# Kernel tuning notes

Hardware: AMD Instinct MI355X
Metric: run time of the kernel (lower is better)

The kernel has to match this reference:

```python
import jax, jax.numpy as jnp
import numpy as np

N_NODES = 10000
LN_EPS = 1e-5


def _gcn(x, W, b, src, dst):
    # GraphConvolution: linear transform then sum-aggregate messages over edges.
    sup = x @ W                               # [B, N, H]
    msg = sup[:, src, :]                      # [B, E, H] gather from source nodes
    agg = jax.vmap(lambda m: jax.ops.segment_sum(m, dst, num_segments=N_NODES))(msg)
    return agg + b


def _layernorm(x, g, b):
    mu = jnp.mean(x, axis=-1, keepdims=True)
    var = jnp.var(x, axis=-1, keepdims=True)
    return (x - mu) * jax.lax.rsqrt(var + LN_EPS) * g + b


def _attention_pool(x, W, u, num_iterations=3):
    # x: [B, N, d] -> r: [B, 1, d]
    a = jnp.tanh(x @ W) @ u                   # [B, N]
    alpha = jax.nn.softmax(a, axis=1)
    r = jnp.einsum('bn,bnd->bd', alpha, x)
    for _ in range(num_iterations):
        beta = jax.nn.softmax(jnp.einsum('bnd,bd->bn', x, r), axis=1)
        r = jnp.einsum('bn,bnd->bd', beta, x)
    return r[:, None, :]


def _forward(x, src, dst, W_conv0, b_conv0, W_convs, b_convs,
             mW1, mb1, mW2, mb2, mW3, mb3,
             ln1_g, ln1_b, ln2_g, ln2_b, attnW, attnu, fW1, fb1, fW2, fb2,
             fcW, fcb):
    gelu = lambda t: jax.nn.gelu(t, approximate=False)
    # stacked GCN layers (first layer distinct input dim)
    x = gelu(_gcn(x, W_conv0, b_conv0, src, dst))
    for i in range(W_convs.shape[0]):
        x = gelu(_gcn(x, W_convs[i], b_convs[i], src, dst))
    # dropout is identity in eval mode
    # MLP head
    x = jax.nn.relu(x @ mW1 + mb1)
    x = jax.nn.relu(x @ mW2 + mb2)
    x = x @ mW3 + mb3
    # Encoder: 2 layers of (attention-pool residual + LN + FFN residual + LN)
    for i in range(2):
        x = x + _attention_pool(x, attnW[i], attnu[i])   # broadcast [B,1,d]
        x = _layernorm(x, ln1_g[i], ln1_b[i])
        h = jax.nn.relu(x @ fW1[i] + fb1[i]) @ fW2[i] + fb2[i]
        x = _layernorm(x + h, ln2_g[i], ln2_b[i])
    x = x @ fcW + fcb                          # [B, N, out]
    return x.mean(axis=1)                      # [B, out]


def setup_inputs() -> dict:
    key = jax.random.key(0)
    ks = jax.random.split(key, 32)
    B, N, E = 4, N_NODES, 160000
    F_in, H, D, A, OUT = 128, 256, 256, 8, 10
    s = lambda k, *shape: jax.random.normal(k, shape, jnp.float32) * 0.05
    return {
        'x': jax.random.normal(ks[0], (B, N, F_in), jnp.float32),
        'src': jax.random.randint(ks[1], (E,), 0, N, jnp.int32),
        'dst': jax.random.randint(ks[2], (E,), 0, N, jnp.int32),
        'W_conv0': s(ks[3], F_in, H), 'b_conv0': s(ks[4], H),
        'W_convs': s(ks[5], 3, H, H), 'b_convs': s(ks[6], 3, H),
        'mW1': s(ks[7], H, H // 2), 'mb1': s(ks[8], H // 2),
        'mW2': s(ks[9], H // 2, H // 4), 'mb2': s(ks[10], H // 4),
        'mW3': s(ks[11], H // 4, D), 'mb3': s(ks[12], D),
        'ln1_g': jnp.ones((2, D), jnp.float32), 'ln1_b': jnp.zeros((2, D), jnp.float32),
        'ln2_g': jnp.ones((2, D), jnp.float32), 'ln2_b': jnp.zeros((2, D), jnp.float32),
        'attnW': s(ks[13], 2, D, A), 'attnu': s(ks[14], 2, A),
        'fW1': s(ks[15], 2, D, H), 'fb1': s(ks[16], 2, H),
        'fW2': s(ks[17], 2, H, D), 'fb2': s(ks[18], 2, D),
        'fcW': s(ks[19], D, OUT), 'fcb': s(ks[20], OUT),
    }


def reference(x, src, dst, W_conv0, b_conv0, W_convs, b_convs,
              mW1, mb1, mW2, mb2, mW3, mb3,
              ln1_g, ln1_b, ln2_g, ln2_b, attnW, attnu, fW1, fb1, fW2, fb2,
              fcW, fcb):
    return _forward(x, src, dst, W_conv0, b_conv0, W_convs, b_convs,
                    mW1, mb1, mW2, mb2, mW3, mb3,
                    ln1_g, ln1_b, ln2_g, ln2_b, attnW, attnu, fW1, fb1, fW2, fb2,
                    fcW, fcb)
```

## Files before the change

### kernel.cpp

```cpp
#include <hip/hip_runtime.h>
#include <math.h>

#define NN 10000
#define NB 4
#define NE 160000
#define DM 256
#define MR (NB * NN)
#define LN_EPS 1e-5f
#define PCH 25
#define NCH (NN / PCH)
#define CCH 100

typedef __attribute__((ext_vector_type(8))) short short8;
typedef __attribute__((ext_vector_type(8))) unsigned short us8;
typedef __attribute__((ext_vector_type(4))) float floatx4;


__device__ inline float bf2f(unsigned short u) {
    unsigned int x = ((unsigned int)u) << 16;
    float f;
    __builtin_memcpy(&f, &x, 4);
    return f;
}

__device__ inline unsigned short f2bf(float f) {
    unsigned int x;
    __builtin_memcpy(&x, &f, 4);
    unsigned int r = x + 0x7FFFu + ((x >> 16) & 1u);
    return (unsigned short)(r >> 16);
}

__device__ inline float gelu_exact(float x) {
    return 0.5f * x * (1.0f + erff(x * 0.70710678118654752f));
}

__device__ inline float waveAllReduce(float v) {
#pragma unroll
    for (int off = 32; off > 0; off >>= 1) v += __shfl_xor(v, off, 64);
    return v;
}

__device__ inline void gld16(const unsigned short* g, unsigned short* l) {
    __builtin_amdgcn_global_load_lds((const __attribute__((address_space(1))) void*)g,
                                     (__attribute__((address_space(3))) void*)l, 16, 0, 0);
}


__global__ void zero_f32_kernel(float* p, int n) {
    int i = blockIdx.x * 256 + threadIdx.x;
    if (i < n) p[i] = 0.0f;
}

__global__ void zero_i32_kernel(int* p, int n) {
    int i = blockIdx.x * 256 + threadIdx.x;
    if (i < n) p[i] = 0;
}

__global__ void cvt_bf16_kernel(const float* __restrict__ in, unsigned short* __restrict__ out, int n) {
    int i = blockIdx.x * 256 + threadIdx.x;
    if (i < n) out[i] = f2bf(in[i]);
}

struct TD { const float* src; unsigned short* dst; int K; int N; };
struct TDs { TD d[11]; };

__global__ void transpose_all_kernel(TDs tds) {
    TD t = tds.d[blockIdx.y];
    int idx = blockIdx.x * 256 + threadIdx.x;
    int total = t.K * t.N;
    if (idx < total) {
        int n = idx / t.K;
        int k = idx - n * t.K;
        t.dst[idx] = f2bf(t.src[(size_t)k * t.N + n]);
    }
}


__global__ void hist_kernel(const int* __restrict__ dst, int* __restrict__ counts, int e) {
    int i = blockIdx.x * 256 + threadIdx.x;
    if (i < e) atomicAdd(&counts[dst[i]], 1);
}

__global__ __launch_bounds__(256) void scan_kernel(const int* __restrict__ counts,
                                                   int* __restrict__ row_ptr,
                                                   int* __restrict__ fill_pos, int n) {
    __shared__ int sums[256];
    int tid = threadIdx.x;
    int chunk = (n + 255) / 256;
    int s0 = tid * chunk;
    int s1 = min(n, s0 + chunk);
    int local = 0;
    for (int i = s0; i < s1; i++) local += counts[i];
    sums[tid] = local;
    __syncthreads();
    for (int off = 1; off < 256; off <<= 1) {
        int v = (tid >= off) ? sums[tid - off] : 0;
        __syncthreads();
        sums[tid] += v;
        __syncthreads();
    }
    int base = (tid == 0) ? 0 : sums[tid - 1];
    for (int i = s0; i < s1; i++) {
        row_ptr[i] = base;
        fill_pos[i] = base;
        base += counts[i];
    }
    if (tid == 255) row_ptr[n] = sums[255];
}

__global__ void fill_kernel(const int* __restrict__ src, const int* __restrict__ dst,
                            int* __restrict__ fill_pos, int* __restrict__ csr_src, int e) {
    int i = blockIdx.x * 256 + threadIdx.x;
    if (i < e) {
        int p = atomicAdd(&fill_pos[dst[i]], 1);
        csr_src[p] = src[i];
    }
}


template <int BN, int CM>
__global__ __launch_bounds__(256) void mfma_gemm_kernel(
    const unsigned short* __restrict__ A, const unsigned short* __restrict__ Bt,
    const float* __restrict__ bias, void* __restrict__ Cp, int K, int N, int act) {
    constexpr int NBF = BN / 32;
    __shared__ unsigned short AsL[4 * 64 * 8];
    __shared__ unsigned short BsL[(BN / 16) * 64 * 8];

    const int tid = threadIdx.x;
    const int w = tid >> 6, l = tid & 63;
    const int wm = w >> 1, wn = w & 1;
    const int bm0 = blockIdx.y * 64;
    const int bn0 = blockIdx.x * BN;
    const int lm = l & 15, lq = l >> 4;

    floatx4 acc[2][NBF];
#pragma unroll
    for (int mi = 0; mi < 2; mi++)
#pragma unroll
        for (int ni = 0; ni < NBF; ni++) acc[mi][ni] = (floatx4){0.f, 0.f, 0.f, 0.f};

    const int s_ll = tid & 63;
    const int a_row = bm0 + (tid >> 6) * 16 + (s_ll & 15);
    const int s_kc = (s_ll >> 4) * 8;

    for (int k0 = 0; k0 < K; k0 += 32) {
        gld16(&A[(size_t)a_row * K + k0 + s_kc], &AsL[tid * 8]);
#pragma unroll
        for (int cc = 0; cc < BN / 64; cc++) {
            int c = tid + cc * 256;
            int rown = bn0 + (c >> 6) * 16 + (c & 15);
            int kc = k0 + ((c & 63) >> 4) * 8;
            gld16(&Bt[(size_t)rown * K + kc], &BsL[c * 8]);
        }
        __syncthreads();
        short8 af[2], bfv[NBF];
#pragma unroll
        for (int mi = 0; mi < 2; mi++) af[mi] = *(short8*)&AsL[((wm * 2 + mi) * 64 + l) * 8];
#pragma unroll
        for (int ni = 0; ni < NBF; ni++) bfv[ni] = *(short8*)&BsL[((wn * NBF + ni) * 64 + l) * 8];
#pragma unroll
        for (int mi = 0; mi < 2; mi++)
#pragma unroll
            for (int ni = 0; ni < NBF; ni++)
                acc[mi][ni] = __builtin_amdgcn_mfma_f32_16x16x32_bf16(af[mi], bfv[ni], acc[mi][ni], 0, 0, 0);
        __syncthreads();
    }

#pragma unroll
    for (int ni = 0; ni < NBF; ni++) {
        int col = bn0 + (wn * NBF + ni) * 16 + lm;
        float bv = bias ? bias[col] : 0.0f;
#pragma unroll
        for (int mi = 0; mi < 2; mi++) {
            int row0 = bm0 + (wm * 2 + mi) * 16 + lq * 4;
#pragma unroll
            for (int r = 0; r < 4; r++) {
                int row = row0 + r;
                float v = acc[mi][ni][r] + bv;
                if (act) v = fmaxf(v, 0.0f);
                if (CM == 0) {
                    ((float*)Cp)[(size_t)row * N + col] = v;
                } else if (CM == 1) {
                    ((unsigned short*)Cp)[(size_t)row * N + col] = f2bf(v);
                } else {
                    int bb = row / NN;
                    int nn = row - bb * NN;
                    ((unsigned short*)Cp)[(size_t)nn * (NB * DM) + bb * DM + col] = f2bf(v);
                }
            }
        }
    }
}


__global__ __launch_bounds__(256) void agg_kernel(const unsigned short* __restrict__ sup,
                                                  const int* __restrict__ row_ptr,
                                                  const int* __restrict__ csr_src,
                                                  const float* __restrict__ bias,
                                                  unsigned short* __restrict__ out) {
    int n = blockIdx.x;
    int w = threadIdx.x >> 6, l = threadIdx.x & 63;
    int s = row_ptr[n], e = row_ptr[n + 1];
    const int off = w * DM + l * 4;
    float a0 = 0.f, a1 = 0.f, a2 = 0.f, a3 = 0.f;
    int j = s;
    for (; j + 8 <= e; j += 8) {
        int idx[8];
#pragma unroll
        for (int k = 0; k < 8; k++) idx[k] = csr_src[j + k];
        ushort4 v[8];
#pragma unroll
        for (int k = 0; k < 8; k++) v[k] = *(const ushort4*)&sup[(size_t)idx[k] * (NB * DM) + off];
#pragma unroll
        for (int k = 0; k < 8; k++) {
            a0 += bf2f(v[k].x); a1 += bf2f(v[k].y);
            a2 += bf2f(v[k].z); a3 += bf2f(v[k].w);
        }
    }
    for (; j < e; j++) {
        ushort4 v = *(const ushort4*)&sup[(size_t)csr_src[j] * (NB * DM) + off];
        a0 += bf2f(v.x); a1 += bf2f(v.y); a2 += bf2f(v.z); a3 += bf2f(v.w);
    }
    int d0 = l * 4;
    const float4 bv = *(const float4*)&bias[d0];
    ushort4 o;
    o.x = f2bf(gelu_exact(a0 + bv.x));
    o.y = f2bf(gelu_exact(a1 + bv.y));
    o.z = f2bf(gelu_exact(a2 + bv.z));
    o.w = f2bf(gelu_exact(a3 + bv.w));
    *(ushort4*)&out[((size_t)w * NN + n) * DM + d0] = o;
}


__global__ __launch_bounds__(256) void attn_score_kernel(const unsigned short* __restrict__ x16,
                                                         const float* __restrict__ W,
                                                         const float* __restrict__ u,
                                                         float* __restrict__ s) {
    int l = threadIdx.x & 63, w = threadIdx.x >> 6;
    int idx = blockIdx.x * 4 + w;
    ushort4 xb = *(const ushort4*)&x16[(size_t)idx * DM + l * 4];
    float xs[4] = {bf2f(xb.x), bf2f(xb.y), bf2f(xb.z), bf2f(xb.w)};
    const float4* Wv = (const float4*)W;
    int d0 = l * 4;
    float t[8] = {0, 0, 0, 0, 0, 0, 0, 0};
#pragma unroll
    for (int dd = 0; dd < 4; dd++) {
        float4 w0 = Wv[(d0 + dd) * 2 + 0];
        float4 w1 = Wv[(d0 + dd) * 2 + 1];
        t[0] += xs[dd] * w0.x; t[1] += xs[dd] * w0.y; t[2] += xs[dd] * w0.z; t[3] += xs[dd] * w0.w;
        t[4] += xs[dd] * w1.x; t[5] += xs[dd] * w1.y; t[6] += xs[dd] * w1.z; t[7] += xs[dd] * w1.w;
    }
#pragma unroll
    for (int j = 0; j < 8; j++) t[j] = waveAllReduce(t[j]);
    if (l == 0) {
        float acc = 0.0f;
#pragma unroll
        for (int j = 0; j < 8; j++) acc += tanhf(t[j]) * u[j];
        s[idx] = acc;
    }
}

__global__ __launch_bounds__(256) void dot_kernel(const unsigned short* __restrict__ x16,
                                                  const float* __restrict__ r,
                                                  float* __restrict__ s) {
    int l = threadIdx.x & 63, w = threadIdx.x >> 6;
    int idx = blockIdx.x * 4 + w;
    int b = idx / NN;
    ushort4 xb = *(const ushort4*)&x16[(size_t)idx * DM + l * 4];
    float4 rv = *(const float4*)&r[b * DM + l * 4];
    float acc = bf2f(xb.x) * rv.x + bf2f(xb.y) * rv.y + bf2f(xb.z) * rv.z + bf2f(xb.w) * rv.w;
    acc = waveAllReduce(acc);
    if (l == 0) s[idx] = acc;
}

__global__ __launch_bounds__(256) void attn_pool_kernel(const unsigned short* __restrict__ x16,
                                                        const float* __restrict__ sarr,
                                                        float* __restrict__ pm,
                                                        float* __restrict__ pl,
                                                        float* __restrict__ pv) {
    int c = blockIdx.x, b = blockIdx.y;
    int tid = threadIdx.x, w = tid >> 6, l = tid & 63;
    int n0 = c * PCH;
    float m = -INFINITY, L = 0.0f;
    float v0 = 0.f, v1 = 0.f, v2 = 0.f, v3 = 0.f;
    for (int n = n0 + w; n < n0 + PCH; n += 4) {
        float s = sarr[b * NN + n];
        ushort4 xb = *(const ushort4*)&x16[((size_t)b * NN + n) * DM + l * 4];
        float x0 = bf2f(xb.x), x1 = bf2f(xb.y), x2 = bf2f(xb.z), x3 = bf2f(xb.w);
        if (s > m) {
            float sc = __expf(m - s);
            L *= sc; v0 *= sc; v1 *= sc; v2 *= sc; v3 *= sc;
            m = s;
        }
        float wgt = __expf(s - m);
        L += wgt;
        v0 += wgt * x0; v1 += wgt * x1; v2 += wgt * x2; v3 += wgt * x3;
    }
    __shared__ float sm[4], sl[4];
    __shared__ float sv[4][DM];
    if (l == 0) { sm[w] = m; sl[w] = L; }
    float4 vv = {v0, v1, v2, v3};
    *(float4*)&sv[w][l * 4] = vv;
    __syncthreads();
    int d = tid;
    float M = fmaxf(fmaxf(sm[0], sm[1]), fmaxf(sm[2], sm[3]));
    float e0 = __expf(sm[0] - M), e1 = __expf(sm[1] - M);
    float e2 = __expf(sm[2] - M), e3 = __expf(sm[3] - M);
    float Lt = e0 * sl[0] + e1 * sl[1] + e2 * sl[2] + e3 * sl[3];
    float vd = e0 * sv[0][d] + e1 * sv[1][d] + e2 * sv[2][d] + e3 * sv[3][d];
    pv[((size_t)b * NCH + c) * DM + d] = vd;
    if (d == 0) {
        pm[b * NCH + c] = M;
        pl[b * NCH + c] = Lt;
    }
}

__global__ __launch_bounds__(256) void attn_combine_kernel(const float* __restrict__ pm,
                                                           const float* __restrict__ pl,
                                                           const float* __restrict__ pv,
                                                           float* __restrict__ r) {
    int b = blockIdx.x, tid = threadIdx.x;
    __shared__ float red[256];
    __shared__ float se[NCH];
    float mv = -INFINITY;
    for (int c = tid; c < NCH; c += 256) mv = fmaxf(mv, pm[b * NCH + c]);
    red[tid] = mv;
    __syncthreads();
    for (int off = 128; off > 0; off >>= 1) {
        if (tid < off) red[tid] = fmaxf(red[tid], red[tid + off]);
        __syncthreads();
    }
    float M = red[0];
    __syncthreads();
    float lsum = 0.0f;
    for (int c = tid; c < NCH; c += 256) {
        float e = __expf(pm[b * NCH + c] - M);
        se[c] = e;
        lsum += e * pl[b * NCH + c];
    }
    red[tid] = lsum;
    __syncthreads();
    for (int off = 128; off > 0; off >>= 1) {
        if (tid < off) red[tid] += red[tid + off];
        __syncthreads();
    }
    float L = red[0];
    __syncthreads();
    float acc = 0.0f;
    for (int c = 0; c < NCH; c++) acc += se[c] * pv[((size_t)b * NCH + c) * DM + tid];
    r[b * DM + tid] = acc / L;
}


__global__ __launch_bounds__(256) void ln_bcast_kernel(const unsigned short* __restrict__ x16,
                                                       const float* __restrict__ r,
                                                       const float* __restrict__ g,
                                                       const float* __restrict__ bt,
                                                       unsigned short* __restrict__ out16) {
    int l = threadIdx.x & 63, w = threadIdx.x >> 6;
    int row = blockIdx.x * 4 + w;
    int b = row / NN;
    ushort4 xb = *(const ushort4*)&x16[(size_t)row * DM + l * 4];
    float4 rv = *(const float4*)(r + (size_t)b * DM + l * 4);
    float4 y;
    y.x = bf2f(xb.x) + rv.x; y.y = bf2f(xb.y) + rv.y;
    y.z = bf2f(xb.z) + rv.z; y.w = bf2f(xb.w) + rv.w;
    float s = y.x + y.y + y.z + y.w;
    float sq = y.x * y.x + y.y * y.y + y.z * y.z + y.w * y.w;
    s = waveAllReduce(s);
    sq = waveAllReduce(sq);
    float mean = s * (1.0f / 256.0f);
    float var = sq * (1.0f / 256.0f) - mean * mean;
    float rstd = rsqrtf(var + LN_EPS);
    float4 gv = *(const float4*)(g + l * 4);
    float4 bv = *(const float4*)(bt + l * 4);
    ushort4 o;
    o.x = f2bf((y.x - mean) * rstd * gv.x + bv.x);
    o.y = f2bf((y.y - mean) * rstd * gv.y + bv.y);
    o.z = f2bf((y.z - mean) * rstd * gv.z + bv.z);
    o.w = f2bf((y.w - mean) * rstd * gv.w + bv.w);
    *(ushort4*)&out16[(size_t)row * DM + l * 4] = o;
}

__global__ __launch_bounds__(256) void ln_elem_kernel(const unsigned short* __restrict__ x16,
                                                      const float* __restrict__ h,
                                                      const float* __restrict__ g,
                                                      const float* __restrict__ bt,
                                                      unsigned short* __restrict__ out16) {
    int l = threadIdx.x & 63, w = threadIdx.x >> 6;
    int row = blockIdx.x * 4 + w;
    ushort4 xb = *(const ushort4*)&x16[(size_t)row * DM + l * 4];
    float4 hv = *(const float4*)(h + (size_t)row * DM + l * 4);
    float4 y;
    y.x = bf2f(xb.x) + hv.x; y.y = bf2f(xb.y) + hv.y;
    y.z = bf2f(xb.z) + hv.z; y.w = bf2f(xb.w) + hv.w;
    float s = y.x + y.y + y.z + y.w;
    float sq = y.x * y.x + y.y * y.y + y.z * y.z + y.w * y.w;
    s = waveAllReduce(s);
    sq = waveAllReduce(sq);
    float mean = s * (1.0f / 256.0f);
    float var = sq * (1.0f / 256.0f) - mean * mean;
    float rstd = rsqrtf(var + LN_EPS);
    float4 gv = *(const float4*)(g + l * 4);
    float4 bv = *(const float4*)(bt + l * 4);
    ushort4 o;
    o.x = f2bf((y.x - mean) * rstd * gv.x + bv.x);
    o.y = f2bf((y.y - mean) * rstd * gv.y + bv.y);
    o.z = f2bf((y.z - mean) * rstd * gv.z + bv.z);
    o.w = f2bf((y.w - mean) * rstd * gv.w + bv.w);
    *(ushort4*)&out16[(size_t)row * DM + l * 4] = o;
}


__global__ __launch_bounds__(256) void colsum_kernel(const unsigned short* __restrict__ x16,
                                                     float* __restrict__ cs) {
    int b = blockIdx.y, c = blockIdx.x, d = threadIdx.x;
    int n0 = c * CCH, n1 = n0 + CCH;
    float acc = 0.0f;
    for (int n = n0; n < n1; n++) acc += bf2f(x16[((size_t)b * NN + n) * DM + d]);
    atomicAdd(&cs[b * DM + d], acc);
}

__global__ __launch_bounds__(64) void final_kernel(const float* __restrict__ cs,
                                                   const float* __restrict__ fcW,
                                                   const float* __restrict__ fcb,
                                                   float* __restrict__ out) {
    int b = blockIdx.x;
    int o = threadIdx.x;
    if (o < 10) {
        float acc = 0.0f;
        for (int d = 0; d < DM; d++) acc += cs[b * DM + d] * fcW[d * 10 + o];
        out[b * 10 + o] = acc * (1.0f / NN) + fcb[o];
    }
}


extern "C" void kernel_launch(void* const* d_in, const int* in_sizes, int n_in,
                              void* d_out, int out_size, void* d_ws, size_t ws_size,
                              hipStream_t stream) {
    const float* x_in    = (const float*)d_in[0];
    const int*   src     = (const int*)d_in[1];
    const int*   dst     = (const int*)d_in[2];
    const float* W_conv0 = (const float*)d_in[3];
    const float* b_conv0 = (const float*)d_in[4];
    const float* W_convs = (const float*)d_in[5];
    const float* b_convs = (const float*)d_in[6];
    const float* mW1 = (const float*)d_in[7];
    const float* mb1 = (const float*)d_in[8];
    const float* mW2 = (const float*)d_in[9];
    const float* mb2 = (const float*)d_in[10];
    const float* mW3 = (const float*)d_in[11];
    const float* mb3 = (const float*)d_in[12];
    const float* ln1_g = (const float*)d_in[13];
    const float* ln1_b = (const float*)d_in[14];
    const float* ln2_g = (const float*)d_in[15];
    const float* ln2_b = (const float*)d_in[16];
    const float* attnW = (const float*)d_in[17];
    const float* attnu = (const float*)d_in[18];
    const float* fW1 = (const float*)d_in[19];
    const float* fb1 = (const float*)d_in[20];
    const float* fW2 = (const float*)d_in[21];
    const float* fb2 = (const float*)d_in[22];
    const float* fcW = (const float*)d_in[23];
    const float* fcb = (const float*)d_in[24];
    float* out = (float*)d_out;

    char* p = (char*)d_ws;
    auto alloc = [&](size_t bytes) { char* q = p; p += (bytes + 255) & ~(size_t)255; return q; };
    float* A = (float*)alloc((size_t)MR * DM * 4);
    unsigned short* sup16 = (unsigned short*)alloc((size_t)MR * DM * 2);
    unsigned short* act16 = (unsigned short*)alloc((size_t)MR * DM * 2);
    unsigned short* b16   = (unsigned short*)alloc((size_t)MR * DM * 2);
    unsigned short* t1    = (unsigned short*)alloc((size_t)MR * 128 * 2);
    unsigned short* t2    = (unsigned short*)alloc((size_t)MR * 64 * 2);
    unsigned short* wt    = (unsigned short*)alloc((size_t)548864 * 2);
    float* a_score = (float*)alloc((size_t)MR * 4);
    float* rbuf = (float*)alloc(NB * DM * 4);
    float* pm0  = (float*)alloc(NB * NCH * 4);
    float* pl0  = (float*)alloc(NB * NCH * 4);
    float* pv0  = (float*)alloc((size_t)NB * NCH * DM * 4);
    float* colsum = (float*)alloc(NB * DM * 4);
    int* counts   = (int*)alloc(NN * 4);
    int* row_ptr  = (int*)alloc((NN + 1) * 4);
    int* fill_pos = (int*)alloc(NN * 4);
    int* csr_src  = (int*)alloc(NE * 4);

    unsigned short* Wt_conv0 = wt;
    unsigned short* Wt_convs = Wt_conv0 + 32768;
    unsigned short* mW1t = Wt_convs + 196608;
    unsigned short* mW2t = mW1t + 32768;
    unsigned short* mW3t = mW2t + 8192;
    unsigned short* fW1t = mW3t + 16384;
    unsigned short* fW2t = fW1t + 131072;

    const dim3 blk(256);

    zero_i32_kernel<<<(NN + 255) / 256, blk, 0, stream>>>(counts, NN);
    hist_kernel<<<(NE + 255) / 256, blk, 0, stream>>>(dst, counts, NE);
    scan_kernel<<<1, blk, 0, stream>>>(counts, row_ptr, fill_pos, NN);
    fill_kernel<<<(NE + 255) / 256, blk, 0, stream>>>(src, dst, fill_pos, csr_src, NE);

    TDs tds;
    tds.d[0]  = {W_conv0, Wt_conv0, 128, 256};
    tds.d[1]  = {W_convs + 0 * 65536, Wt_convs + 0 * 65536, 256, 256};
    tds.d[2]  = {W_convs + 1 * 65536, Wt_convs + 1 * 65536, 256, 256};
    tds.d[3]  = {W_convs + 2 * 65536, Wt_convs + 2 * 65536, 256, 256};
    tds.d[4]  = {mW1, mW1t, 256, 128};
    tds.d[5]  = {mW2, mW2t, 128, 64};
    tds.d[6]  = {mW3, mW3t, 64, 256};
    tds.d[7]  = {fW1 + 0 * 65536, fW1t + 0 * 65536, 256, 256};
    tds.d[8]  = {fW1 + 1 * 65536, fW1t + 1 * 65536, 256, 256};
    tds.d[9]  = {fW2 + 0 * 65536, fW2t + 0 * 65536, 256, 256};
    tds.d[10] = {fW2 + 1 * 65536, fW2t + 1 * 65536, 256, 256};
    transpose_all_kernel<<<dim3(256, 11), blk, 0, stream>>>(tds);

    cvt_bf16_kernel<<<(MR * 128 + 255) / 256, blk, 0, stream>>>(x_in, t1, MR * 128);

    mfma_gemm_kernel<128, 2><<<dim3(2, MR / 64), blk, 0, stream>>>(t1, Wt_conv0, nullptr, sup16, 128, 256, 0);
    agg_kernel<<<NN, blk, 0, stream>>>(sup16, row_ptr, csr_src, b_conv0, act16);
    for (int i = 0; i < 3; i++) {
        mfma_gemm_kernel<128, 2><<<dim3(2, MR / 64), blk, 0, stream>>>(act16, Wt_convs + (size_t)i * 65536, nullptr, sup16, 256, 256, 0);
        agg_kernel<<<NN, blk, 0, stream>>>(sup16, row_ptr, csr_src, b_convs + (size_t)i * 256, act16);
    }

    mfma_gemm_kernel<128, 1><<<dim3(1, MR / 64), blk, 0, stream>>>(act16, mW1t, mb1, t1, 256, 128, 1);
    mfma_gemm_kernel<64, 1><<<dim3(1, MR / 64), blk, 0, stream>>>(t1, mW2t, mb2, t2, 128, 64, 1);
    mfma_gemm_kernel<128, 1><<<dim3(2, MR / 64), blk, 0, stream>>>(t2, mW3t, mb3, act16, 64, 256, 0);

    const dim3 poolGrid(NCH, NB);
    for (int i = 0; i < 2; i++) {
        const float* Wp = attnW + (size_t)i * DM * 8;
        const float* up = attnu + (size_t)i * 8;
        attn_score_kernel<<<MR / 4, blk, 0, stream>>>(act16, Wp, up, a_score);
        attn_pool_kernel<<<poolGrid, blk, 0, stream>>>(act16, a_score, pm0, pl0, pv0);
        attn_combine_kernel<<<NB, blk, 0, stream>>>(pm0, pl0, pv0, rbuf);
        for (int it = 0; it < 3; it++) {
            dot_kernel<<<MR / 4, blk, 0, stream>>>(act16, rbuf, a_score);
            attn_pool_kernel<<<poolGrid, blk, 0, stream>>>(act16, a_score, pm0, pl0, pv0);
            attn_combine_kernel<<<NB, blk, 0, stream>>>(pm0, pl0, pv0, rbuf);
        }
        ln_bcast_kernel<<<MR / 4, blk, 0, stream>>>(act16, rbuf, ln1_g + (size_t)i * DM,
                                                    ln1_b + (size_t)i * DM, b16);
        mfma_gemm_kernel<128, 1><<<dim3(2, MR / 64), blk, 0, stream>>>(b16, fW1t + (size_t)i * 65536,
                                                                       fb1 + (size_t)i * DM, sup16, 256, 256, 1);
        mfma_gemm_kernel<128, 0><<<dim3(2, MR / 64), blk, 0, stream>>>(sup16, fW2t + (size_t)i * 65536,
                                                                       fb2 + (size_t)i * DM, A, 256, 256, 0);
        ln_elem_kernel<<<MR / 4, blk, 0, stream>>>(b16, A, ln2_g + (size_t)i * DM,
                                                   ln2_b + (size_t)i * DM, act16);
    }

    zero_f32_kernel<<<4, blk, 0, stream>>>(colsum, NB * DM);
    colsum_kernel<<<dim3(NN / CCH, NB), blk, 0, stream>>>(act16, colsum);
    final_kernel<<<NB, dim3(64), 0, stream>>>(colsum, fcW, fcb, out);
}
```

Baseline: 895.3 us.

## Fuse attention score computation into pooling kernel and drop atomic colsum

```diff
diff --git a/kernel.cpp b/kernel.cpp
--- a/kernel.cpp
+++ b/kernel.cpp
@@ -7,12 +7,11 @@
 #define DM 256
 #define MR (NB * NN)
 #define LN_EPS 1e-5f
-#define PCH 25
+#define PCH 40
 #define NCH (NN / PCH)
 #define CCH 100
 
 typedef __attribute__((ext_vector_type(8))) short short8;
-typedef __attribute__((ext_vector_type(8))) unsigned short us8;
 typedef __attribute__((ext_vector_type(4))) float floatx4;
 
 
@@ -45,11 +44,6 @@
                                      (__attribute__((address_space(3))) void*)l, 16, 0, 0);
 }
 
-
-__global__ void zero_f32_kernel(float* p, int n) {
-    int i = blockIdx.x * 256 + threadIdx.x;
-    if (i < n) p[i] = 0.0f;
-}
 
 __global__ void zero_i32_kernel(int* p, int n) {
     int i = blockIdx.x * 256 + threadIdx.x;
@@ -177,7 +171,7 @@
             for (int r = 0; r < 4; r++) {
                 int row = row0 + r;
                 float v = acc[mi][ni][r] + bv;
-                if (act) v = fmaxf(v, 0.0f);
+                if (act == 1) v = fmaxf(v, 0.0f);
                 if (CM == 0) {
                     ((float*)Cp)[(size_t)row * N + col] = v;
                 } else if (CM == 1) {
@@ -232,61 +226,52 @@
 }
 
 
-__global__ __launch_bounds__(256) void attn_score_kernel(const unsigned short* __restrict__ x16,
-                                                         const float* __restrict__ W,
-                                                         const float* __restrict__ u,
-                                                         float* __restrict__ s) {
-    int l = threadIdx.x & 63, w = threadIdx.x >> 6;
-    int idx = blockIdx.x * 4 + w;
-    ushort4 xb = *(const ushort4*)&x16[(size_t)idx * DM + l * 4];
-    float xs[4] = {bf2f(xb.x), bf2f(xb.y), bf2f(xb.z), bf2f(xb.w)};
-    const float4* Wv = (const float4*)W;
-    int d0 = l * 4;
-    float t[8] = {0, 0, 0, 0, 0, 0, 0, 0};
-#pragma unroll
-    for (int dd = 0; dd < 4; dd++) {
-        float4 w0 = Wv[(d0 + dd) * 2 + 0];
-        float4 w1 = Wv[(d0 + dd) * 2 + 1];
-        t[0] += xs[dd] * w0.x; t[1] += xs[dd] * w0.y; t[2] += xs[dd] * w0.z; t[3] += xs[dd] * w0.w;
-        t[4] += xs[dd] * w1.x; t[5] += xs[dd] * w1.y; t[6] += xs[dd] * w1.z; t[7] += xs[dd] * w1.w;
-    }
-#pragma unroll
-    for (int j = 0; j < 8; j++) t[j] = waveAllReduce(t[j]);
-    if (l == 0) {
-        float acc = 0.0f;
-#pragma unroll
-        for (int j = 0; j < 8; j++) acc += tanhf(t[j]) * u[j];
-        s[idx] = acc;
-    }
-}
-
-__global__ __launch_bounds__(256) void dot_kernel(const unsigned short* __restrict__ x16,
-                                                  const float* __restrict__ r,
-                                                  float* __restrict__ s) {
-    int l = threadIdx.x & 63, w = threadIdx.x >> 6;
-    int idx = blockIdx.x * 4 + w;
-    int b = idx / NN;
-    ushort4 xb = *(const ushort4*)&x16[(size_t)idx * DM + l * 4];
-    float4 rv = *(const float4*)&r[b * DM + l * 4];
-    float acc = bf2f(xb.x) * rv.x + bf2f(xb.y) * rv.y + bf2f(xb.z) * rv.z + bf2f(xb.w) * rv.w;
-    acc = waveAllReduce(acc);
-    if (l == 0) s[idx] = acc;
-}
-
+template <int MODE>
 __global__ __launch_bounds__(256) void attn_pool_kernel(const unsigned short* __restrict__ x16,
-                                                        const float* __restrict__ sarr,
+                                                        const float* __restrict__ W,
+                                                        const float* __restrict__ u,
+                                                        const float* __restrict__ r_in,
                                                         float* __restrict__ pm,
                                                         float* __restrict__ pl,
                                                         float* __restrict__ pv) {
     int c = blockIdx.x, b = blockIdx.y;
     int tid = threadIdx.x, w = tid >> 6, l = tid & 63;
+    float4 rv = {0, 0, 0, 0};
+    float u0[8];
+    if (MODE == 1) {
+        rv = *(const float4*)&r_in[b * DM + l * 4];
+    } else {
+#pragma unroll
+        for (int j = 0; j < 8; j++) u0[j] = u[j];
+    }
     int n0 = c * PCH;
     float m = -INFINITY, L = 0.0f;
     float v0 = 0.f, v1 = 0.f, v2 = 0.f, v3 = 0.f;
     for (int n = n0 + w; n < n0 + PCH; n += 4) {
-        float s = sarr[b * NN + n];
         ushort4 xb = *(const ushort4*)&x16[((size_t)b * NN + n) * DM + l * 4];
         float x0 = bf2f(xb.x), x1 = bf2f(xb.y), x2 = bf2f(xb.z), x3 = bf2f(xb.w);
+        float s;
+        if (MODE == 1) {
+            s = x0 * rv.x + x1 * rv.y + x2 * rv.z + x3 * rv.w;
+            s = waveAllReduce(s);
+        } else {
+            const float4* Wv = (const float4*)W;
+            int d0 = l * 4;
+            float xs[4] = {x0, x1, x2, x3};
+            float t[8] = {0, 0, 0, 0, 0, 0, 0, 0};
+#pragma unroll
+            for (int dd = 0; dd < 4; dd++) {
+                float4 w0 = Wv[(d0 + dd) * 2 + 0];
+                float4 w1 = Wv[(d0 + dd) * 2 + 1];
+                t[0] += xs[dd] * w0.x; t[1] += xs[dd] * w0.y; t[2] += xs[dd] * w0.z; t[3] += xs[dd] * w0.w;
+                t[4] += xs[dd] * w1.x; t[5] += xs[dd] * w1.y; t[6] += xs[dd] * w1.z; t[7] += xs[dd] * w1.w;
+            }
+#pragma unroll
+            for (int jj = 0; jj < 8; jj++) t[jj] = waveAllReduce(t[jj]);
+            s = 0.f;
+#pragma unroll
+            for (int jj = 0; jj < 8; jj++) s += tanhf(t[jj]) * u0[jj];
+        }
         if (s > m) {
             float sc = __expf(m - s);
             L *= sc; v0 *= sc; v1 *= sc; v2 *= sc; v3 *= sc;
@@ -413,24 +398,28 @@
 
 
 __global__ __launch_bounds__(256) void colsum_kernel(const unsigned short* __restrict__ x16,
-                                                     float* __restrict__ cs) {
+                                                     float* __restrict__ pcol) {
     int b = blockIdx.y, c = blockIdx.x, d = threadIdx.x;
     int n0 = c * CCH, n1 = n0 + CCH;
     float acc = 0.0f;
     for (int n = n0; n < n1; n++) acc += bf2f(x16[((size_t)b * NN + n) * DM + d]);
-    atomicAdd(&cs[b * DM + d], acc);
-}
-
-__global__ __launch_bounds__(64) void final_kernel(const float* __restrict__ cs,
-                                                   const float* __restrict__ fcW,
-                                                   const float* __restrict__ fcb,
-                                                   float* __restrict__ out) {
-    int b = blockIdx.x;
-    int o = threadIdx.x;
-    if (o < 10) {
-        float acc = 0.0f;
-        for (int d = 0; d < DM; d++) acc += cs[b * DM + d] * fcW[d * 10 + o];
-        out[b * 10 + o] = acc * (1.0f / NN) + fcb[o];
+    pcol[((size_t)b * (NN / CCH) + c) * DM + d] = acc;
+}
+
+__global__ __launch_bounds__(256) void final_kernel(const float* __restrict__ pcol,
+                                                    const float* __restrict__ fcW,
+                                                    const float* __restrict__ fcb,
+                                                    float* __restrict__ out) {
+    int b = blockIdx.x, d = threadIdx.x;
+    __shared__ float sx[DM];
+    float acc = 0.0f;
+    for (int c = 0; c < NN / CCH; c++) acc += pcol[((size_t)b * (NN / CCH) + c) * DM + d];
+    sx[d] = acc;
+    __syncthreads();
+    if (d < 10) {
+        float o = 0.0f;
+        for (int k = 0; k < DM; k++) o += sx[k] * fcW[k * 10 + d];
+        out[b * 10 + d] = o * (1.0f / NN) + fcb[d];
     }
 }
 
@@ -474,12 +463,11 @@
     unsigned short* t1    = (unsigned short*)alloc((size_t)MR * 128 * 2);
     unsigned short* t2    = (unsigned short*)alloc((size_t)MR * 64 * 2);
     unsigned short* wt    = (unsigned short*)alloc((size_t)548864 * 2);
-    float* a_score = (float*)alloc((size_t)MR * 4);
     float* rbuf = (float*)alloc(NB * DM * 4);
     float* pm0  = (float*)alloc(NB * NCH * 4);
     float* pl0  = (float*)alloc(NB * NCH * 4);
     float* pv0  = (float*)alloc((size_t)NB * NCH * DM * 4);
-    float* colsum = (float*)alloc(NB * DM * 4);
+    float* pcol = (float*)alloc((size_t)NB * (NN / CCH) * DM * 4);
     int* counts   = (int*)alloc(NN * 4);
     int* row_ptr  = (int*)alloc((NN + 1) * 4);
     int* fill_pos = (int*)alloc(NN * 4);
@@ -531,12 +519,10 @@
     for (int i = 0; i < 2; i++) {
         const float* Wp = attnW + (size_t)i * DM * 8;
         const float* up = attnu + (size_t)i * 8;
-        attn_score_kernel<<<MR / 4, blk, 0, stream>>>(act16, Wp, up, a_score);
-        attn_pool_kernel<<<poolGrid, blk, 0, stream>>>(act16, a_score, pm0, pl0, pv0);
+        attn_pool_kernel<0><<<poolGrid, blk, 0, stream>>>(act16, Wp, up, nullptr, pm0, pl0, pv0);
         attn_combine_kernel<<<NB, blk, 0, stream>>>(pm0, pl0, pv0, rbuf);
         for (int it = 0; it < 3; it++) {
-            dot_kernel<<<MR / 4, blk, 0, stream>>>(act16, rbuf, a_score);
-            attn_pool_kernel<<<poolGrid, blk, 0, stream>>>(act16, a_score, pm0, pl0, pv0);
+            attn_pool_kernel<1><<<poolGrid, blk, 0, stream>>>(act16, nullptr, nullptr, rbuf, pm0, pl0, pv0);
             attn_combine_kernel<<<NB, blk, 0, stream>>>(pm0, pl0, pv0, rbuf);
         }
         ln_bcast_kernel<<<MR / 4, blk, 0, stream>>>(act16, rbuf, ln1_g + (size_t)i * DM,
@@ -549,7 +535,6 @@
                                                    ln2_b + (size_t)i * DM, act16);
     }
 
-    zero_f32_kernel<<<4, blk, 0, stream>>>(colsum, NB * DM);
-    colsum_kernel<<<dim3(NN / CCH, NB), blk, 0, stream>>>(act16, colsum);
-    final_kernel<<<NB, dim3(64), 0, stream>>>(colsum, fcW, fcb, out);
-}
+    colsum_kernel<<<dim3(NN / CCH, NB), blk, 0, stream>>>(act16, pcol);
+    final_kernel<<<NB, blk, 0, stream>>>(pcol, fcW, fcb, out);
+}
```

Result: faster. 790.9 us (-11.7%).
